# Kernel optimization log

Measured on AMD Instinct MI355X. Metric: run time of the kernel, lower is better.

The kernel has to match this reference:

```python
import jax, jax.numpy as jnp
import numpy as np

B, IN_DIM, HV_DIM, NUM_CLASSES = 16384, 2048, 8192, 1000


def setup_inputs() -> dict:
    key = jax.random.key(0)
    kx, kp, kc = jax.random.split(key, 3)
    x = jax.random.normal(kx, (B, IN_DIM), dtype=jnp.float32)
    # +/-1 random projection and class hypervectors (2*bernoulli - 1), as in the torch buffers
    proj = (jax.random.randint(kp, (IN_DIM, HV_DIM), 0, 2) * 2 - 1).astype(jnp.float32)
    class_hv = (jax.random.randint(kc, (HV_DIM, NUM_CLASSES), 0, 2) * 2 - 1).astype(jnp.float32)
    return {"x": x, "proj": proj, "class_hv": class_hv}


def reference(x, proj, class_hv):
    # dense projection -> sign binarize -> binary associative-memory matmul (score_mode='dot')
    hv = x @ proj                                   # [B, HV_DIM]
    hv_bin = jnp.where(hv >= 0, 1.0, -1.0).astype(hv.dtype)
    scores = hv_bin @ class_hv                      # [B, NUM_CLASSES]
    return scores, hv_bin
```

## Files before the change

### kernel.cpp

```cpp
#include <hip/hip_runtime.h>
#include <hip/hip_bf16.h>

typedef _Float16 half8  __attribute__((ext_vector_type(8)));
typedef _Float16 half4_t __attribute__((ext_vector_type(4)));
typedef float    floatx4 __attribute__((ext_vector_type(4)));
typedef int      intx4   __attribute__((ext_vector_type(4)));

#define B_DIM   16384
#define IN_D    2048
#define HV_D    8192
#define NC      1000
#define NCP     1024
#define SCORES_N (B_DIM * NC)

#define GLD16(gp, lp) __builtin_amdgcn_global_load_lds( \
    (const __attribute__((address_space(1))) void*)(gp), \
    (__attribute__((address_space(3))) void*)(lp), 16, 0, 0)

__global__ void k_split(const float* __restrict__ x, _Float16* __restrict__ xh,
                        _Float16* __restrict__ xl) {
    size_t i = (size_t)blockIdx.x * 256 + threadIdx.x;
    floatx4 v = ((const floatx4*)x)[i];
    half4_t h, l;
#pragma unroll
    for (int j = 0; j < 4; ++j) {
        _Float16 hh = (_Float16)v[j];
        h[j] = hh;
        l[j] = (_Float16)(v[j] - (float)hh);
    }
    ((half4_t*)xh)[i] = h;
    ((half4_t*)xl)[i] = l;
}

__global__ void k_transpose_proj(const float* __restrict__ p, _Float16* __restrict__ pT) {
    __shared__ float tile[64][65];
    const int t = threadIdx.x;
    const int nt = blockIdx.x * 64;
    const int kt = blockIdx.y * 64;
    const int tr = t >> 4, tc = (t & 15) * 4;
#pragma unroll
    for (int s = 0; s < 4; ++s) {
        int r = tr + s * 16;
        floatx4 v = *(const floatx4*)&p[(size_t)(kt + r) * HV_D + nt + tc];
        tile[r][tc] = v[0]; tile[r][tc + 1] = v[1];
        tile[r][tc + 2] = v[2]; tile[r][tc + 3] = v[3];
    }
    __syncthreads();
#pragma unroll
    for (int s = 0; s < 4; ++s) {
        int rn = tr + s * 16;
        half4_t o;
#pragma unroll
        for (int j = 0; j < 4; ++j) o[j] = (_Float16)tile[tc + j][rn];
        *(half4_t*)&pT[(size_t)(nt + rn) * IN_D + kt + tc] = o;
    }
}

__global__ void k_pack_class(const float* __restrict__ c, signed char* __restrict__ cT) {
    __shared__ signed char tile[64][68];
    const int t = threadIdx.x;
    const int nt = blockIdx.x * 64;
    const int kt = blockIdx.y * 64;
    const int nl = t & 63;
    const int n = nt + nl;
#pragma unroll
    for (int s = 0; s < 16; ++s) {
        const int kl = s * 4 + (t >> 6);
        signed char v = 0;
        if (n < NC) {
            float f = c[(size_t)(kt + kl) * NC + n];
            v = (f >= 0.f) ? (signed char)1 : (signed char)-1;
        }
        tile[kl][nl] = v;
    }
    __syncthreads();
    const int wn = t >> 2;
    const int wk = (t & 3) * 16;
    intx4 o;
    signed char* ob = (signed char*)&o;
#pragma unroll
    for (int j = 0; j < 16; ++j) ob[j] = tile[wk + j][wn];
    *(intx4*)&cT[(size_t)(nt + wn) * HV_D + kt + wk] = o;
}

__launch_bounds__(256, 2)
__global__ void k_gemm1(const _Float16* __restrict__ xh, const _Float16* __restrict__ xl,
                        const _Float16* __restrict__ pT,
                        float* __restrict__ hv_out, signed char* __restrict__ hvb,
                        int mbase) {
    __shared__ _Float16 sAh[128 * 64];
    __shared__ _Float16 sAl[128 * 64];
    __shared__ _Float16 sB [256 * 64];
    const int t = threadIdx.x;
    const int w = t >> 6, l = t & 63;

    const int orig = blockIdx.y * 32 + blockIdx.x;
    const int lid  = (orig & 7) * 128 + (orig >> 3);
    const int bx = lid & 31, by = lid >> 5;

    const int m0 = mbase + by * 128, n0 = bx * 256;
    const int wm = (w >> 1) * 64, wn = (w & 1) * 128;
    const int lm = l & 15, kq = l >> 4;
    const int srow  = w * 8 + (l >> 3);
    const int scol  = (((l & 7) ^ ((l >> 3) & 7))) * 8;
    const int sbyte = w * 1024 + l * 16;

    floatx4 acc[4][8] = {};

    for (int k0 = 0; k0 < IN_D; k0 += 64) {
        __syncthreads();
#pragma unroll
        for (int i = 0; i < 4; ++i) {
            const size_t ga = (size_t)(m0 + srow + i * 32) * IN_D + k0 + scol;
            const int lo = sbyte + i * 4096;
            GLD16(xh + ga, (char*)sAh + lo);
            GLD16(xl + ga, (char*)sAl + lo);
        }
#pragma unroll
        for (int i = 0; i < 8; ++i) {
            const size_t gb = (size_t)(n0 + srow + i * 32) * IN_D + k0 + scol;
            GLD16(pT + gb, (char*)sB + sbyte + i * 4096);
        }
        __syncthreads();
#pragma unroll
        for (int ks = 0; ks < 2; ++ks) {
            const int csw = ((ks * 4 + kq) ^ (lm & 7)) * 8;
            half8 b[8];
#pragma unroll
            for (int ns = 0; ns < 8; ++ns)
                b[ns] = *(const half8*)&sB[(wn + ns * 16 + lm) * 64 + csw];
#pragma unroll
            for (int ms = 0; ms < 4; ++ms) {
                half8 a = *(const half8*)&sAh[(wm + ms * 16 + lm) * 64 + csw];
#pragma unroll
                for (int ns = 0; ns < 8; ++ns)
                    acc[ms][ns] = __builtin_amdgcn_mfma_f32_16x16x32_f16(a, b[ns], acc[ms][ns], 0, 0, 0);
            }
#pragma unroll
            for (int ms = 0; ms < 4; ++ms) {
                half8 a = *(const half8*)&sAl[(wm + ms * 16 + lm) * 64 + csw];
#pragma unroll
                for (int ns = 0; ns < 8; ++ns)
                    acc[ms][ns] = __builtin_amdgcn_mfma_f32_16x16x32_f16(a, b[ns], acc[ms][ns], 0, 0, 0);
            }
        }
    }

#pragma unroll
    for (int ms = 0; ms < 4; ++ms) {
#pragma unroll
        for (int ns = 0; ns < 8; ++ns) {
            const int m = m0 + wm + ms * 16 + kq * 4;
            const int n = n0 + wn + ns * 16 + lm;
#pragma unroll
            for (int r = 0; r < 4; ++r) {
                const int pos = (acc[ms][ns][r] >= 0.f);
                const size_t o = (size_t)(m + r) * HV_D + n;
                __builtin_nontemporal_store(pos ? 1.f : -1.f, &hv_out[o]);
                hvb[o] = (signed char)(pos ? 1 : -1);
            }
        }
    }
}

__launch_bounds__(256, 4)
__global__ void k_gemm2(const signed char* __restrict__ hvb, const signed char* __restrict__ cT,
                        float* __restrict__ scores) {
    __shared__ signed char sA[64 * 128];
    __shared__ signed char sB[256 * 128];
    const int t = threadIdx.x;
    const int w = t >> 6, l = t & 63;

    const int orig = blockIdx.y * 4 + blockIdx.x;
    const int lid  = (orig & 7) * 128 + (orig >> 3);
    const int bx = lid & 3, by = lid >> 2;

    const int m0 = by * 64, n0 = bx * 256;
    const int wm = (w >> 1) * 32, wn = (w & 1) * 128;
    const int lm = l & 15, kq = l >> 4;
    const int srow  = w * 8 + (l >> 3);
    const int scol  = (((l & 7) ^ ((l >> 3) & 7))) * 16;
    const int sbyte = w * 1024 + l * 16;

    intx4 acc[2][8] = {};

    for (int k0 = 0; k0 < HV_D; k0 += 128) {
        __syncthreads();
#pragma unroll
        for (int i = 0; i < 2; ++i)
            GLD16(hvb + (size_t)(m0 + srow + i * 32) * HV_D + k0 + scol,
                  (char*)sA + sbyte + i * 4096);
#pragma unroll
        for (int i = 0; i < 8; ++i)
            GLD16(cT + (size_t)(n0 + srow + i * 32) * HV_D + k0 + scol,
                  (char*)sB + sbyte + i * 4096);
        __syncthreads();
#pragma unroll
        for (int ks = 0; ks < 2; ++ks) {
            const int csw = ((ks * 4 + kq) ^ (lm & 7)) * 16;
            intx4 b[8];
#pragma unroll
            for (int ns = 0; ns < 8; ++ns)
                b[ns] = *(const intx4*)&sB[(wn + ns * 16 + lm) * 128 + csw];
#pragma unroll
            for (int ms = 0; ms < 2; ++ms) {
                intx4 a = *(const intx4*)&sA[(wm + ms * 16 + lm) * 128 + csw];
#pragma unroll
                for (int ns = 0; ns < 8; ++ns)
                    acc[ms][ns] = __builtin_amdgcn_mfma_i32_16x16x64_i8(a, b[ns], acc[ms][ns], 0, 0, 0);
            }
        }
    }

#pragma unroll
    for (int ms = 0; ms < 2; ++ms) {
#pragma unroll
        for (int ns = 0; ns < 8; ++ns) {
            const int m = m0 + wm + ms * 16 + kq * 4;
            const int n = n0 + wn + ns * 16 + lm;
            if (n < NC) {
#pragma unroll
                for (int r = 0; r < 4; ++r)
                    __builtin_nontemporal_store((float)acc[ms][ns][r],
                                                &scores[(size_t)(m + r) * NC + n]);
            }
        }
    }
}

extern "C" void kernel_launch(void* const* d_in, const int* in_sizes, int n_in,
                              void* d_out, int out_size, void* d_ws, size_t ws_size,
                              hipStream_t stream) {
    const float* x    = (const float*)d_in[0];
    const float* proj = (const float*)d_in[1];
    const float* chv  = (const float*)d_in[2];
    float* out    = (float*)d_out;
    float* scores = out;
    float* hv_out = out + (size_t)SCORES_N;

    char* ws = (char*)d_ws;
    _Float16*    xh  = (_Float16*)(ws);
    _Float16*    xl  = (_Float16*)(ws + (size_t)67108864);
    _Float16*    pT  = (_Float16*)(ws + (size_t)134217728);
    signed char* cT  = (signed char*)(ws + (size_t)167772160);
    signed char* hvb = (signed char*)(ws + (size_t)176160768);

    k_split<<<(B_DIM * IN_D / 4) / 256, 256, 0, stream>>>(x, xh, xl);
    k_transpose_proj<<<dim3(HV_D / 64, IN_D / 64), 256, 0, stream>>>(proj, pT);
    k_pack_class<<<dim3(NCP / 64, HV_D / 64), 256, 0, stream>>>(chv, cT);
    k_gemm1<<<dim3(HV_D / 256, B_DIM / 512), 256, 0, stream>>>(xh, xl, pT, hv_out, hvb, 0);
    k_gemm1<<<dim3(HV_D / 256, B_DIM / 512), 256, 0, stream>>>(xh, xl, pT, hv_out, hvb, 4096);
    k_gemm1<<<dim3(HV_D / 256, B_DIM / 512), 256, 0, stream>>>(xh, xl, pT, hv_out, hvb, 8192);
    k_gemm1<<<dim3(HV_D / 256, B_DIM / 512), 256, 0, stream>>>(xh, xl, pT, hv_out, hvb, 12288);
    k_gemm2<<<dim3(NCP / 256, B_DIM / 64), 256, 0, stream>>>(hvb, cT, scores);
}
```

Baseline: 1.697 ms.

## Double-buffer gemm2 LDS loads, drop gemm1 swizzle, use two gemm1 launches

The int8 class-score GEMM now uses two LDS buffers, so global-to-LDS loads for the next K tile are issued before computing the current one. Waits are handled with explicit vmcnt and barriers. Its occupancy hint drops from 4 to 2 blocks because LDS use doubles. Separately, gemm1 loses its block-index remap, switches hv output to regular stores instead of nontemporal, and is launched as two halves instead of four quarters. That may change L2 locality for the projection GEMM.

```diff
diff --git a/kernel.cpp b/kernel.cpp
--- a/kernel.cpp
+++ b/kernel.cpp
@@ -93,12 +93,7 @@
     __shared__ _Float16 sB [256 * 64];
     const int t = threadIdx.x;
     const int w = t >> 6, l = t & 63;
-
-    const int orig = blockIdx.y * 32 + blockIdx.x;
-    const int lid  = (orig & 7) * 128 + (orig >> 3);
-    const int bx = lid & 31, by = lid >> 5;
-
-    const int m0 = mbase + by * 128, n0 = bx * 256;
+    const int m0 = mbase + blockIdx.y * 128, n0 = blockIdx.x * 256;
     const int wm = (w >> 1) * 64, wn = (w & 1) * 128;
     const int lm = l & 15, kq = l >> 4;
     const int srow  = w * 8 + (l >> 3);
@@ -156,18 +151,18 @@
             for (int r = 0; r < 4; ++r) {
                 const int pos = (acc[ms][ns][r] >= 0.f);
                 const size_t o = (size_t)(m + r) * HV_D + n;
-                __builtin_nontemporal_store(pos ? 1.f : -1.f, &hv_out[o]);
+                hv_out[o] = pos ? 1.f : -1.f;
                 hvb[o] = (signed char)(pos ? 1 : -1);
             }
         }
     }
 }
 
-__launch_bounds__(256, 4)
+__launch_bounds__(256, 2)
 __global__ void k_gemm2(const signed char* __restrict__ hvb, const signed char* __restrict__ cT,
                         float* __restrict__ scores) {
-    __shared__ signed char sA[64 * 128];
-    __shared__ signed char sB[256 * 128];
+    __shared__ signed char sA[2][64 * 128];
+    __shared__ signed char sB[2][256 * 128];
     const int t = threadIdx.x;
     const int w = t >> 6, l = t & 63;
 
@@ -184,33 +179,58 @@
 
     intx4 acc[2][8] = {};
 
-    for (int k0 = 0; k0 < HV_D; k0 += 128) {
-        __syncthreads();
-#pragma unroll
-        for (int i = 0; i < 2; ++i)
-            GLD16(hvb + (size_t)(m0 + srow + i * 32) * HV_D + k0 + scol,
-                  (char*)sA + sbyte + i * 4096);
-#pragma unroll
-        for (int i = 0; i < 8; ++i)
-            GLD16(cT + (size_t)(n0 + srow + i * 32) * HV_D + k0 + scol,
-                  (char*)sB + sbyte + i * 4096);
-        __syncthreads();
-#pragma unroll
-        for (int ks = 0; ks < 2; ++ks) {
-            const int csw = ((ks * 4 + kq) ^ (lm & 7)) * 16;
-            intx4 b[8];
-#pragma unroll
-            for (int ns = 0; ns < 8; ++ns)
-                b[ns] = *(const intx4*)&sB[(wn + ns * 16 + lm) * 128 + csw];
-#pragma unroll
-            for (int ms = 0; ms < 2; ++ms) {
-                intx4 a = *(const intx4*)&sA[(wm + ms * 16 + lm) * 128 + csw];
-#pragma unroll
-                for (int ns = 0; ns < 8; ++ns)
-                    acc[ms][ns] = __builtin_amdgcn_mfma_i32_16x16x64_i8(a, b[ns], acc[ms][ns], 0, 0, 0);
-            }
-        }
-    }
+#define G2_STAGE(buf, kt) do { \
+    const int k0_ = (kt) * 128; \
+    _Pragma("unroll") \
+    for (int i = 0; i < 2; ++i) \
+        GLD16(hvb + (size_t)(m0 + srow + i * 32) * HV_D + k0_ + scol, \
+              (char*)&sA[buf][0] + sbyte + i * 4096); \
+    _Pragma("unroll") \
+    for (int i = 0; i < 8; ++i) \
+        GLD16(cT + (size_t)(n0 + srow + i * 32) * HV_D + k0_ + scol, \
+              (char*)&sB[buf][0] + sbyte + i * 4096); \
+} while (0)
+
+#define G2_COMPUTE(buf) do { \
+    _Pragma("unroll") \
+    for (int ks = 0; ks < 2; ++ks) { \
+        const int csw = ((ks * 4 + kq) ^ (lm & 7)) * 16; \
+        intx4 b[8]; \
+        _Pragma("unroll") \
+        for (int ns = 0; ns < 8; ++ns) \
+            b[ns] = *(const intx4*)&sB[buf][(wn + ns * 16 + lm) * 128 + csw]; \
+        _Pragma("unroll") \
+        for (int ms = 0; ms < 2; ++ms) { \
+            intx4 a = *(const intx4*)&sA[buf][(wm + ms * 16 + lm) * 128 + csw]; \
+            _Pragma("unroll") \
+            for (int ns = 0; ns < 8; ++ns) \
+                acc[ms][ns] = __builtin_amdgcn_mfma_i32_16x16x64_i8(a, b[ns], acc[ms][ns], 0, 0, 0); \
+        } \
+    } \
+} while (0)
+
+    G2_STAGE(0, 0);
+
+#pragma unroll 1
+    for (int kt = 0; kt < 63; ++kt) {
+        const int cur = kt & 1;
+        __builtin_amdgcn_s_barrier();
+        if (cur == 0) G2_STAGE(1, kt + 1); else G2_STAGE(0, kt + 1);
+        asm volatile("s_waitcnt vmcnt(10)" ::: "memory");
+        __builtin_amdgcn_sched_barrier(0);
+        __builtin_amdgcn_s_barrier();
+        __builtin_amdgcn_sched_barrier(0);
+        if (cur == 0) G2_COMPUTE(0); else G2_COMPUTE(1);
+    }
+    __builtin_amdgcn_s_barrier();
+    asm volatile("s_waitcnt vmcnt(0)" ::: "memory");
+    __builtin_amdgcn_sched_barrier(0);
+    __builtin_amdgcn_s_barrier();
+    __builtin_amdgcn_sched_barrier(0);
+    G2_COMPUTE(1);
+
+#undef G2_STAGE
+#undef G2_COMPUTE
 
 #pragma unroll
     for (int ms = 0; ms < 2; ++ms) {
@@ -248,9 +268,7 @@
     k_split<<<(B_DIM * IN_D / 4) / 256, 256, 0, stream>>>(x, xh, xl);
     k_transpose_proj<<<dim3(HV_D / 64, IN_D / 64), 256, 0, stream>>>(proj, pT);
     k_pack_class<<<dim3(NCP / 64, HV_D / 64), 256, 0, stream>>>(chv, cT);
-    k_gemm1<<<dim3(HV_D / 256, B_DIM / 512), 256, 0, stream>>>(xh, xl, pT, hv_out, hvb, 0);
-    k_gemm1<<<dim3(HV_D / 256, B_DIM / 512), 256, 0, stream>>>(xh, xl, pT, hv_out, hvb, 4096);
-    k_gemm1<<<dim3(HV_D / 256, B_DIM / 512), 256, 0, stream>>>(xh, xl, pT, hv_out, hvb, 8192);
-    k_gemm1<<<dim3(HV_D / 256, B_DIM / 512), 256, 0, stream>>>(xh, xl, pT, hv_out, hvb, 12288);
+    k_gemm1<<<dim3(HV_D / 256, B_DIM / 256), 256, 0, stream>>>(xh, xl, pT, hv_out, hvb, 0);
+    k_gemm1<<<dim3(HV_D / 256, B_DIM / 256), 256, 0, stream>>>(xh, xl, pT, hv_out, hvb, B_DIM / 2);
     k_gemm2<<<dim3(NCP / 256, B_DIM / 64), 256, 0, stream>>>(hvb, cT, scores);
 }
```

Result: faster. 1.661 ms (-2.1%).
